# Optimization experiments

Measured on AMD Instinct MI355X. Metric: run time of the kernel, lower is better.

Reference implementation:

```python
import jax, jax.numpy as jnp
import numpy as np

B, T, DM, DH, DD, V, K = 2, 512, 1024, 4096, 4, 32000, 8
THR = 0.25
EPS = 1e-5
IGN = -100


def setup_inputs() -> dict:
    key = jax.random.key(0)
    ks = jax.random.split(key, 12)
    s = 0.02
    return {
        "H": jax.random.normal(ks[0], (B, T, DM), jnp.float32),
        "input_ids": jax.random.randint(ks[1], (B, T), 0, V),
        "attention_mask": jax.random.randint(ks[2], (B, T), 0, 2),
        "labels": jax.random.randint(ks[3], (B, T), 0, V),
        "emb": s * jax.random.normal(ks[4], (V, DM), jnp.float32),
        "depth_emb": s * jax.random.normal(ks[5], (DD, DM), jnp.float32),
        "ln_g": jnp.ones((DM,), jnp.float32),
        "ln_b": jnp.zeros((DM,), jnp.float32),
        "W1": s * jax.random.normal(ks[6], (DM, DH), jnp.float32),
        "b1": jnp.zeros((DH,), jnp.float32),
        "W2": s * jax.random.normal(ks[7], (DH, DM), jnp.float32),
        "b2": jnp.zeros((DM,), jnp.float32),
        "Wq": s * jax.random.normal(ks[8], (DM, V), jnp.float32),
        "bq": jnp.zeros((V,), jnp.float32),
        "Wb": s * jax.random.normal(ks[9], (DM, 1), jnp.float32),
        "bb": jnp.zeros((1,), jnp.float32),
    }


def _forward(H, input_ids, attention_mask, labels, emb, depth_emb, ln_g, ln_b, W1, b1, W2, b2, Wq, bq, Wb, bb):
    mask = attention_mask.astype(bool)  # (B,T)
    E = emb[input_ids]  # (B,T,DM)
    # draft state: broadcast over depth dim
    S = H[:, :, None, :] + E[:, :, None, :] + depth_emb[None, None]  # (B,T,DD,DM)
    mu = S.mean(-1, keepdims=True)
    var = ((S - mu) ** 2).mean(-1, keepdims=True)  # biased var, as torch LayerNorm
    S = (S - mu) * jax.lax.rsqrt(var + EPS) * ln_g + ln_b
    S = jax.nn.gelu(S @ W1 + b1, approximate=False) @ W2 + b2
    q = S @ Wq + bq  # (B,T,DD,V)
    beta = (S @ Wb + bb)[..., 0]  # (B,T,DD)
    q = jnp.where(mask[:, :, None, None], q, 0.0)
    beta = jnp.where(mask[:, :, None], beta, 0.0)
    # future labels for D depths (small fixed loop over DD)
    targets = jnp.full((B, T, DD), IGN, jnp.int32)
    valid = jnp.zeros((B, T, DD), bool)
    for d in range(1, DD + 1):
        v = mask[:, : T - d] & mask[:, d:]
        valid = valid.at[:, : T - d, d - 1].set(v)
        targets = targets.at[:, : T - d, d - 1].set(
            jnp.where(v, labels[:, d:].astype(jnp.int32), IGN))
    # token CE over valid positions (masked mean)
    logp = jax.nn.log_softmax(q, axis=-1)
    safe = jnp.where(valid, targets, 0)
    nll = -jnp.take_along_axis(logp, safe[..., None], axis=-1)[..., 0]
    cnt = valid.sum()
    L_q = jnp.where(cnt > 0, (nll * valid).sum() / jnp.maximum(cnt, 1).astype(q.dtype), jnp.zeros((), q.dtype))
    # BCE-with-logits on beta, averaged over valid source positions
    bce = jnp.logaddexp(0.0, beta) - beta * valid.astype(beta.dtype)
    src = valid.any(-1, keepdims=True)
    denom = jnp.maximum(src.sum(), 1).astype(beta.dtype)
    L_beta = (bce * src).sum() / denom
    return q, beta, L_q + L_beta


def reference(H, input_ids, attention_mask, labels, emb, depth_emb, ln_g, ln_b, W1, b1, W2, b2, Wq, bq, Wb, bb):
    q, beta, loss = _forward(H, input_ids, attention_mask, labels, emb, depth_emb,
                             ln_g, ln_b, W1, b1, W2, b2, Wq, bq, Wb, bb)
    # dynamic_branch_width
    sigma = jax.nn.sigmoid(beta)
    k = jnp.clip(jnp.ceil(sigma * float(K)).astype(jnp.int32), 1, K)
    k = jnp.where(sigma >= THR, k, 0)
    k = jnp.where(attention_mask.astype(bool)[:, :, None], k, 0)
    return q, beta, k, loss
```

## Files before the change

kernel.cpp:

```cpp
#include <hip/hip_runtime.h>
#include <math.h>

#define B_ 2
#define T_ 512
#define DM_ 1024
#define DH_ 4096
#define DD_ 4
#define V_ 32000
#define M_ 4096
#define BT_ 1024
#define NCHUNK3_ 125
#define PCH_ 128

typedef __attribute__((ext_vector_type(8))) unsigned short ushort8_t;
typedef __attribute__((ext_vector_type(4))) unsigned short ushort4_t;
typedef __attribute__((ext_vector_type(8))) __bf16 bf16x8;
typedef __attribute__((ext_vector_type(4))) float f32x4;

__device__ __forceinline__ unsigned short f2bf(float x) {
  union { float f; unsigned u; } v; v.f = x;
  unsigned r = v.u + 0x7fffu + ((v.u >> 16) & 1u);
  return (unsigned short)(r >> 16);
}
__device__ __forceinline__ float bf2f(unsigned short h) {
  union { unsigned u; float f; } v; v.u = ((unsigned)h) << 16; return v.f;
}

__device__ __forceinline__ void gload16(const void* g, void* l) {
  __builtin_amdgcn_global_load_lds(
      (const __attribute__((address_space(1))) void*)g,
      (__attribute__((address_space(3))) void*)l, 16, 0, 0);
}

template<int ROWS, int NWAVE>
__device__ __forceinline__ void stage_swz(const unsigned short* __restrict__ src, int ld,
                                          unsigned short* lds, int wid, int lane) {
  constexpr int NLOAD = ROWS / (16 * NWAVE);
  const int rl = lane >> 2;
  const int slot = (lane & 3) ^ ((lane >> 3) & 3);
  #pragma unroll
  for (int i = 0; i < NLOAD; ++i) {
    const int rbase = (i * NWAVE + wid) * 16;
    gload16(src + (size_t)(rbase + rl) * ld + slot * 8, lds + rbase * 32);
  }
}

__device__ __forceinline__ bf16x8 ldfrag(const unsigned short* t, int r, int s) {
  return __builtin_bit_cast(bf16x8,
      *(const ushort8_t*)&t[r * 32 + ((s ^ ((r >> 1) & 3)) * 8)]);
}

__device__ __forceinline__ float block_sum256(float v, float* sh) {
  #pragma unroll
  for (int o = 32; o >= 1; o >>= 1) v += __shfl_down(v, o);
  int lane = threadIdx.x & 63, wid = threadIdx.x >> 6;
  if (lane == 0) sh[wid] = v;
  __syncthreads();
  float t = sh[0] + sh[1] + sh[2] + sh[3];
  __syncthreads();
  return t;
}

__global__ __launch_bounds__(256) void transpose_split_kernel(
    const float* __restrict__ in, int R, int C,
    unsigned short* __restrict__ out_hi, unsigned short* __restrict__ out_lo)
{
  __shared__ float tile[32][33];
  int c0 = blockIdx.x * 32, r0 = blockIdx.y * 32;
  int tx = threadIdx.x & 31, ty = threadIdx.x >> 5;
  #pragma unroll
  for (int i = 0; i < 4; ++i)
    tile[ty + i * 8][tx] = in[(size_t)(r0 + ty + i * 8) * C + c0 + tx];
  __syncthreads();
  #pragma unroll
  for (int i = 0; i < 4; ++i) {
    int orow = c0 + ty + i * 8;
    int ocol = r0 + tx;
    float v = tile[tx][ty + i * 8];
    unsigned short h = f2bf(v);
    out_hi[(size_t)orow * R + ocol] = h;
    if (out_lo) out_lo[(size_t)orow * R + ocol] = f2bf(v - bf2f(h));
  }
}

__global__ __launch_bounds__(256) void embed_ln_kernel(
    const float* __restrict__ H, const int* __restrict__ ids,
    const float* __restrict__ emb, const float* __restrict__ demb,
    const float* __restrict__ g, const float* __restrict__ be,
    unsigned short* __restrict__ Xhi, unsigned short* __restrict__ Xlo)
{
  __shared__ float sh[8];
  int m = blockIdx.x, tid = threadIdx.x;
  int bt = m >> 2, d = m & 3;
  int id = ids[bt];
  float4 x  = ((const float4*)(H   + (size_t)bt * DM_))[tid];
  float4 e  = ((const float4*)(emb + (size_t)id * DM_))[tid];
  float4 de = ((const float4*)(demb + (size_t)d * DM_))[tid];
  float v0 = x.x + e.x + de.x, v1 = x.y + e.y + de.y;
  float v2 = x.z + e.z + de.z, v3 = x.w + e.w + de.w;
  float mu = block_sum256((v0 + v1) + (v2 + v3), sh) * (1.0f / DM_);
  float d0 = v0 - mu, d1v = v1 - mu, d2 = v2 - mu, d3 = v3 - mu;
  float var = block_sum256((d0 * d0 + d1v * d1v) + (d2 * d2 + d3 * d3), sh) * (1.0f / DM_);
  float rs = rsqrtf(var + 1e-5f);
  float4 gg  = ((const float4*)g)[tid];
  float4 bb4 = ((const float4*)be)[tid];
  float y0 = d0 * rs * gg.x + bb4.x;
  float y1 = d1v * rs * gg.y + bb4.y;
  float y2 = d2 * rs * gg.z + bb4.z;
  float y3 = d3 * rs * gg.w + bb4.w;
  unsigned short h0 = f2bf(y0), h1 = f2bf(y1), h2 = f2bf(y2), h3 = f2bf(y3);
  ushort4_t hv = {h0, h1, h2, h3};
  ushort4_t lv = {f2bf(y0 - bf2f(h0)), f2bf(y1 - bf2f(h1)), f2bf(y2 - bf2f(h2)), f2bf(y3 - bf2f(h3))};
  size_t base = (size_t)m * DM_ + tid * 4;
  *(ushort4_t*)&Xhi[base] = hv;
  *(ushort4_t*)&Xlo[base] = lv;
}

__global__ __launch_bounds__(64) void w2b_kernel(
    const float* __restrict__ W2, const float* __restrict__ Wb,
    const float* __restrict__ b2, const float* __restrict__ bb,
    float* __restrict__ w2b)
{
  int j = blockIdx.x, lane = threadIdx.x;
  const float* rowp = (j < DH_) ? (W2 + (size_t)j * DM_) : b2;
  const float4* r4 = (const float4*)rowp;
  const float4* w4 = (const float4*)Wb;
  float s = 0.0f;
  for (int i = lane; i < DM_ / 4; i += 64) {
    float4 a = r4[i], w = w4[i];
    s += a.x * w.x + a.y * w.y + a.z * w.z + a.w * w.w;
  }
  #pragma unroll
  for (int o = 32; o >= 1; o >>= 1) s += __shfl_down(s, o);
  if (lane == 0) w2b[j] = (j < DH_) ? s : (s + bb[0]);
}

template<int BM, int BN, int NWAVE, int WN,
         bool SPLIT, bool GELU, bool CEPART, bool BETAPART, bool NTC>
__global__ __launch_bounds__(NWAVE * 64, 2) void gemm3p_kernel(
    const unsigned short* __restrict__ Ahi, const unsigned short* __restrict__ Alo,
    const unsigned short* __restrict__ Bhi, const unsigned short* __restrict__ Blo,
    const float* __restrict__ bias, int Ndim, int Kdim,
    float* __restrict__ Cf, unsigned short* __restrict__ Chi, unsigned short* __restrict__ Clo,
    const int* __restrict__ rowmask,
    const float* __restrict__ w2bv, float* __restrict__ bpart,
    float* __restrict__ pmax, float* __restrict__ psum)
{
  constexpr int WM = NWAVE / WN;
  constexpr int MI = (BM / WM) / 16;
  constexpr int NI = (BN / WN) / 16;
  constexpr int AW = BM * 32;
  constexpr int BW = BN * 32;
  constexpr int BUFW = (SPLIT ? 2 : 1) * (AW + BW);
  constexpr int LPS = (SPLIT ? 2 : 1) * (BM / (16 * NWAVE) + BN / (16 * NWAVE));
  static_assert(LPS == 4, "vmcnt(4) assumes exactly 4 loads per wave per stage");
  __shared__ __align__(16) unsigned short smem[3 * BUFW];

  const int m0 = blockIdx.x * BM, n0 = blockIdx.y * BN;
  const int tid = threadIdx.x, lane = tid & 63, wid = tid >> 6;
  const int wr = wid / WN, wc = wid % WN;
  const int lrow = lane & 15, q4 = lane >> 4;
  const int wrb = wr * (BM / WM), wcb = wc * (BN / WN);

  const unsigned short* Ab  = Ahi + (size_t)m0 * Kdim;
  const unsigned short* Bb  = Bhi + (size_t)n0 * Kdim;
  const unsigned short* Alb = SPLIT ? (Alo + (size_t)m0 * Kdim) : nullptr;
  const unsigned short* Blb = SPLIT ? (Blo + (size_t)n0 * Kdim) : nullptr;

  f32x4 acc[MI][NI] = {};
  const int NT = Kdim / 32;

  auto stageAll = [&](unsigned short* base, int kt) {
    const int ko = kt * 32;
    stage_swz<BM, NWAVE>(Ab + ko, Kdim, base, wid, lane);
    stage_swz<BN, NWAVE>(Bb + ko, Kdim, base + AW, wid, lane);
    if constexpr (SPLIT) {
      stage_swz<BM, NWAVE>(Alb + ko, Kdim, base + AW + BW, wid, lane);
      stage_swz<BN, NWAVE>(Blb + ko, Kdim, base + 2 * AW + BW, wid, lane);
    }
  };

  unsigned short* p0 = smem;
  unsigned short* p1 = smem + BUFW;
  unsigned short* p2 = smem + 2 * BUFW;

  stageAll(p0, 0);
  stageAll(p1, 1);

  for (int kt = 0; kt < NT; ++kt) {
    if (kt + 1 < NT) asm volatile("s_waitcnt vmcnt(4)" ::: "memory");
    else             asm volatile("s_waitcnt vmcnt(0)" ::: "memory");
    __builtin_amdgcn_s_barrier();
    __builtin_amdgcn_sched_barrier(0);
    if (kt + 2 < NT) stageAll(p2, kt + 2);
    __builtin_amdgcn_sched_barrier(0);

    const unsigned short* sA = p0;
    const unsigned short* sB = p0 + AW;
    bf16x8 bh[NI], bl[NI];
    #pragma unroll
    for (int ni = 0; ni < NI; ++ni) {
      bh[ni] = ldfrag(sB, wcb + ni * 16 + lrow, q4);
      if constexpr (SPLIT) bl[ni] = ldfrag(sB + AW + BW, wcb + ni * 16 + lrow, q4);
    }
    #pragma unroll
    for (int mi = 0; mi < MI; ++mi) {
      const int r = wrb + mi * 16 + lrow;
      bf16x8 ah = ldfrag(sA, r, q4);
      bf16x8 al;
      if constexpr (SPLIT) al = ldfrag(sA + AW + BW, r, q4);
      #pragma unroll
      for (int ni = 0; ni < NI; ++ni) {
        acc[mi][ni] = __builtin_amdgcn_mfma_f32_16x16x32_bf16(ah, bh[ni], acc[mi][ni], 0, 0, 0);
        if constexpr (SPLIT) {
          acc[mi][ni] = __builtin_amdgcn_mfma_f32_16x16x32_bf16(ah, bl[ni], acc[mi][ni], 0, 0, 0);
          acc[mi][ni] = __builtin_amdgcn_mfma_f32_16x16x32_bf16(al, bh[ni], acc[mi][ni], 0, 0, 0);
        }
      }
    }
    unsigned short* t = p0; p0 = p1; p1 = p2; p2 = t;
  }
  __syncthreads();

  #pragma unroll
  for (int mi = 0; mi < MI; ++mi)
    #pragma unroll
    for (int ni = 0; ni < NI; ++ni) {
      const int col = n0 + wcb + ni * 16 + lrow;
      const float bv = bias ? bias[col] : 0.0f;
      #pragma unroll
      for (int r2 = 0; r2 < 4; ++r2) {
        const int gm = m0 + wrb + mi * 16 + q4 * 4 + r2;
        float v = acc[mi][ni][r2] + bv;
        if constexpr (GELU) v = 0.5f * v * (1.0f + erff(v * 0.70710678118654752440f));
        if (rowmask) v *= (rowmask[gm >> 2] ? 1.0f : 0.0f);
        acc[mi][ni][r2] = v;
        const size_t idx = (size_t)gm * Ndim + col;
        if (Cf) {
          if constexpr (NTC) __builtin_nontemporal_store(v, &Cf[idx]);
          else Cf[idx] = v;
        }
        if (Chi) {
          unsigned short h = f2bf(v);
          Chi[idx] = h;
          if (Clo) Clo[idx] = f2bf(v - bf2f(h));
        }
      }
    }

  float* red = (float*)smem;

  if constexpr (CEPART) {
    #pragma unroll
    for (int mi = 0; mi < MI; ++mi)
      #pragma unroll
      for (int r2 = 0; r2 < 4; ++r2) {
        float mx = -3.4e38f;
        #pragma unroll
        for (int ni = 0; ni < NI; ++ni) mx = fmaxf(mx, acc[mi][ni][r2]);
        #pragma unroll
        for (int o = 1; o < 16; o <<= 1) mx = fmaxf(mx, __shfl_xor(mx, o));
        float sm = 0.0f;
        #pragma unroll
        for (int ni = 0; ni < NI; ++ni) sm += expf(acc[mi][ni][r2] - mx);
        #pragma unroll
        for (int o = 1; o < 16; o <<= 1) sm += __shfl_xor(sm, o);
        if (lrow == 0) {
          const int rowL = wrb + mi * 16 + q4 * 4 + r2;
          red[(rowL * WN + wc) * 2 + 0] = mx;
          red[(rowL * WN + wc) * 2 + 1] = sm;
        }
      }
    __syncthreads();
    for (int r = tid; r < BM; r += NWAVE * 64) {
      float mg = -3.4e38f, sg = 0.0f;
      #pragma unroll
      for (int w = 0; w < WN; ++w) {
        float mw = red[(r * WN + w) * 2 + 0], sw = red[(r * WN + w) * 2 + 1];
        float nm = fmaxf(mg, mw);
        sg = sg * expf(mg - nm) + sw * expf(mw - nm);
        mg = nm;
      }
      pmax[(size_t)(m0 + r) * PCH_ + blockIdx.y] = mg;
      psum[(size_t)(m0 + r) * PCH_ + blockIdx.y] = sg;
    }
  }

  if constexpr (BETAPART) {
    #pragma unroll
    for (int mi = 0; mi < MI; ++mi)
      #pragma unroll
      for (int r2 = 0; r2 < 4; ++r2) {
        float s = 0.0f;
        #pragma unroll
        for (int ni = 0; ni < NI; ++ni)
          s += acc[mi][ni][r2] * w2bv[n0 + wcb + ni * 16 + lrow];
        #pragma unroll
        for (int o = 1; o < 16; o <<= 1) s += __shfl_xor(s, o);
        if (lrow == 0)
          red[(wrb + mi * 16 + q4 * 4 + r2) * WN + wc] = s;
      }
    __syncthreads();
    for (int r = tid; r < BM; r += NWAVE * 64) {
      float s = 0.0f;
      #pragma unroll
      for (int w = 0; w < WN; ++w) s += red[r * WN + w];
      bpart[(size_t)(m0 + r) * 32 + blockIdx.y] = s;
    }
  }
}

__global__ __launch_bounds__(64) void beta_k_kernel(
    const float* __restrict__ bpart, const float* __restrict__ w2b,
    const int* __restrict__ mask,
    float* __restrict__ beta_out, float* __restrict__ k_out,
    float* __restrict__ bce, int* __restrict__ validf)
{
  int m = blockIdx.x, lane = threadIdx.x;
  float s = (lane < 32) ? bpart[(size_t)m * 32 + lane] : 0.0f;
  #pragma unroll
  for (int o = 32; o >= 1; o >>= 1) s += __shfl_down(s, o);
  if (lane == 0) {
    int bt = m >> 2, d1 = (m & 3) + 1;
    float beta = s + w2b[DH_];
    int mv = mask[bt];
    float bm = mv ? beta : 0.0f;
    int t = bt % T_;
    int valid = (t + d1 < T_) && mv && mask[bt + d1];
    beta_out[m] = bm;
    float sp = fmaxf(bm, 0.0f) + log1pf(expf(-fabsf(bm)));
    bce[m] = sp - (valid ? bm : 0.0f);
    validf[m] = valid;
    float sig = 1.0f / (1.0f + expf(-bm));
    int kk = (int)ceilf(sig * 8.0f);
    kk = kk < 1 ? 1 : (kk > 8 ? 8 : kk);
    if (!(sig >= 0.25f)) kk = 0;
    if (!mv) kk = 0;
    k_out[m] = (float)kk;
  }
}

__global__ __launch_bounds__(64) void ce_reduce_kernel(
    const float* __restrict__ pmax, const float* __restrict__ psum,
    const float* __restrict__ q, const int* __restrict__ validf,
    const int* __restrict__ labels, float* __restrict__ nll)
{
  int m = blockIdx.x, lane = threadIdx.x;
  if (!validf[m]) { if (lane == 0) nll[m] = 0.0f; return; }
  float ml = -3.4e38f, sl = 0.0f;
  for (int j = lane; j < NCHUNK3_; j += 64) {
    float mj = pmax[(size_t)m * PCH_ + j], sj = psum[(size_t)m * PCH_ + j];
    float nm = fmaxf(ml, mj);
    sl = sl * expf(ml - nm) + sj * expf(mj - nm);
    ml = nm;
  }
  #pragma unroll
  for (int o = 32; o >= 1; o >>= 1) {
    float mo = __shfl_xor(ml, o), so = __shfl_xor(sl, o);
    float nm = fmaxf(ml, mo);
    sl = sl * expf(ml - nm) + so * expf(mo - nm);
    ml = nm;
  }
  if (lane == 0) {
    int bt = m >> 2, d1 = (m & 3) + 1;
    float qt = q[(size_t)m * V_ + labels[bt + d1]];
    nll[m] = -(qt - ml - logf(sl));
  }
}

__global__ __launch_bounds__(256) void loss_kernel(
    const float* __restrict__ nll, const int* __restrict__ validf,
    const float* __restrict__ bce, float* __restrict__ loss_out)
{
  __shared__ float sh[8];
  int tid = threadIdx.x;
  float snll = 0.0f, fcnt = 0.0f, sbce = 0.0f, fnsrc = 0.0f;
  for (int m = tid; m < M_; m += 256) { snll += nll[m]; fcnt += (float)validf[m]; }
  for (int bt = tid; bt < BT_; bt += 256) {
    int base = bt * 4;
    int src = validf[base] | validf[base + 1] | validf[base + 2] | validf[base + 3];
    if (src) { sbce += bce[base] + bce[base + 1] + bce[base + 2] + bce[base + 3]; fnsrc += 1.0f; }
  }
  snll = block_sum256(snll, sh);
  fcnt = block_sum256(fcnt, sh);
  sbce = block_sum256(sbce, sh);
  fnsrc = block_sum256(fnsrc, sh);
  if (tid == 0) {
    float Lq = fcnt > 0.0f ? snll / fcnt : 0.0f;
    float Lb = sbce / fmaxf(fnsrc, 1.0f);
    loss_out[0] = Lq + Lb;
  }
}

extern "C" void kernel_launch(void* const* d_in, const int* in_sizes, int n_in,
                              void* d_out, int out_size, void* d_ws, size_t ws_size,
                              hipStream_t stream) {
  const float* H    = (const float*)d_in[0];
  const int*   ids  = (const int*)d_in[1];
  const int*   mask = (const int*)d_in[2];
  const int*   labels = (const int*)d_in[3];
  const float* emb  = (const float*)d_in[4];
  const float* demb = (const float*)d_in[5];
  const float* ln_g = (const float*)d_in[6];
  const float* ln_b = (const float*)d_in[7];
  const float* W1   = (const float*)d_in[8];
  const float* b1   = (const float*)d_in[9];
  const float* W2   = (const float*)d_in[10];
  const float* b2   = (const float*)d_in[11];
  const float* Wq   = (const float*)d_in[12];
  const float* bq   = (const float*)d_in[13];
  const float* Wb   = (const float*)d_in[14];
  const float* bb   = (const float*)d_in[15];

  char* ws = (char*)d_ws; size_t off = 0;
  auto walloc = [&](size_t bytes) -> void* {
    void* p = ws + off; off = (off + bytes + 255) & ~(size_t)255; return p;
  };
  unsigned short* W1t_hi = (unsigned short*)walloc((size_t)DH_ * DM_ * 2);
  unsigned short* W1t_lo = (unsigned short*)walloc((size_t)DH_ * DM_ * 2);
  unsigned short* W2t_hi = (unsigned short*)walloc((size_t)DM_ * DH_ * 2);
  unsigned short* Wqt_hi = (unsigned short*)walloc((size_t)V_ * DM_ * 2);
  unsigned short* Xhi    = (unsigned short*)walloc((size_t)M_ * DM_ * 2);
  unsigned short* Xlo    = (unsigned short*)walloc((size_t)M_ * DM_ * 2);
  unsigned short* S2hi   = (unsigned short*)walloc((size_t)M_ * DM_ * 2);
  float* w2b    = (float*)walloc((DH_ + 1) * 4);
  float* bpart  = (float*)walloc((size_t)M_ * 32 * 4);
  float* pmax   = (float*)walloc((size_t)M_ * PCH_ * 4);
  float* psum   = (float*)walloc((size_t)M_ * PCH_ * 4);
  float* nll    = (float*)walloc(M_ * 4);
  float* bcev   = (float*)walloc(M_ * 4);
  int*   validf = (int*)walloc(M_ * 4);

  float* q_out    = (float*)d_out;
  float* beta_out = q_out + (size_t)M_ * V_;
  float* k_out    = beta_out + M_;
  float* loss_out = k_out + M_;
  unsigned short* act_hi = (unsigned short*)d_out;
  unsigned short* act_lo = act_hi + (size_t)M_ * DH_;

  transpose_split_kernel<<<dim3(DH_ / 32, DM_ / 32), 256, 0, stream>>>(W1, DM_, DH_, W1t_hi, W1t_lo);
  transpose_split_kernel<<<dim3(DM_ / 32, DH_ / 32), 256, 0, stream>>>(W2, DH_, DM_, W2t_hi, nullptr);
  transpose_split_kernel<<<dim3(V_ / 32, DM_ / 32), 256, 0, stream>>>(Wq, DM_, V_, Wqt_hi, nullptr);
  embed_ln_kernel<<<M_, 256, 0, stream>>>(H, ids, emb, demb, ln_g, ln_b, Xhi, Xlo);
  w2b_kernel<<<DH_ + 1, 64, 0, stream>>>(W2, Wb, b2, bb, w2b);
  gemm3p_kernel<128, 128, 8, 4, true, true, false, true, false>
      <<<dim3(M_ / 128, DH_ / 128), 512, 0, stream>>>(
      Xhi, Xlo, W1t_hi, W1t_lo, b1, DH_, DM_, nullptr, act_hi, act_lo, nullptr,
      w2b, bpart, nullptr, nullptr);
  beta_k_kernel<<<M_, 64, 0, stream>>>(bpart, w2b, mask, beta_out, k_out, bcev, validf);
  gemm3p_kernel<128, 128, 4, 2, false, false, false, false, false>
      <<<dim3(M_ / 128, DM_ / 128), 256, 0, stream>>>(
      act_hi, nullptr, W2t_hi, nullptr, b2, DM_, DH_, nullptr, S2hi, nullptr, nullptr,
      nullptr, nullptr, nullptr, nullptr);
  gemm3p_kernel<256, 256, 8, 4, false, false, true, false, true>
      <<<dim3(M_ / 256, V_ / 256), 512, 0, stream>>>(
      S2hi, nullptr, Wqt_hi, nullptr, bq, V_, DM_, q_out, nullptr, nullptr, mask,
      nullptr, nullptr, pmax, psum);
  ce_reduce_kernel<<<M_, 64, 0, stream>>>(pmax, psum, q_out, validf, labels, nll);
  loss_kernel<<<1, 256, 0, stream>>>(nll, validf, bcev, loss_out);
}
```

Before: 1.392 ms.

## Add 8-phase ping-pong GEMM kernel with split-precision as concatenated K

Adds a new 256x256-tile GEMM kernel that interleaves LDS fragment loads, global-to-LDS staging and MFMA groups across eight barrier-separated phases, using s_setprio to favour MFMA issue. It is used for the vocabulary projection and for the first MLP layer. The first layer's three-product split-bf16 scheme is now written as one GEMM over a threefold-longer K dimension built from segment pointers (Xhi·W1hi, Xhi·W1lo, Xlo·W1hi) rather than three MFMAs per step. The beta partial-sum reduction is narrowed to 16 column blocks to match the wider tile. The aim is better MFMA utilisation and latency hiding, at the cost of a rigid hand-written schedule with many barriers that assumes a fixed 1024-wide K segment.

```diff
diff --git a/kernel.cpp b/kernel.cpp
--- a/kernel.cpp
+++ b/kernel.cpp
@@ -11,6 +11,7 @@
 #define BT_ 1024
 #define NCHUNK3_ 125
 #define PCH_ 128
+#define NB1_ 16
 
 typedef __attribute__((ext_vector_type(8))) unsigned short ushort8_t;
 typedef __attribute__((ext_vector_type(4))) unsigned short ushort4_t;
@@ -30,24 +31,6 @@
   __builtin_amdgcn_global_load_lds(
       (const __attribute__((address_space(1))) void*)g,
       (__attribute__((address_space(3))) void*)l, 16, 0, 0);
-}
-
-template<int ROWS, int NWAVE>
-__device__ __forceinline__ void stage_swz(const unsigned short* __restrict__ src, int ld,
-                                          unsigned short* lds, int wid, int lane) {
-  constexpr int NLOAD = ROWS / (16 * NWAVE);
-  const int rl = lane >> 2;
-  const int slot = (lane & 3) ^ ((lane >> 3) & 3);
-  #pragma unroll
-  for (int i = 0; i < NLOAD; ++i) {
-    const int rbase = (i * NWAVE + wid) * 16;
-    gload16(src + (size_t)(rbase + rl) * ld + slot * 8, lds + rbase * 32);
-  }
-}
-
-__device__ __forceinline__ bf16x8 ldfrag(const unsigned short* t, int r, int s) {
-  return __builtin_bit_cast(bf16x8,
-      *(const ushort8_t*)&t[r * 32 + ((s ^ ((r >> 1) & 3)) * 8)]);
 }
 
 __device__ __forceinline__ float block_sum256(float v, float* sh) {
@@ -60,6 +43,7 @@
   __syncthreads();
   return t;
 }
+
 
 __global__ __launch_bounds__(256) void transpose_split_kernel(
     const float* __restrict__ in, int R, int C,
@@ -135,25 +119,39 @@
   if (lane == 0) w2b[j] = (j < DH_) ? s : (s + bb[0]);
 }
 
-template<int BM, int BN, int NWAVE, int WN,
-         bool SPLIT, bool GELU, bool CEPART, bool BETAPART, bool NTC>
+
+template<int ROWS, int NWAVE>
+__device__ __forceinline__ void stage_swz(const unsigned short* __restrict__ src, int ld,
+                                          unsigned short* lds, int wid, int lane) {
+  constexpr int NLOAD = ROWS / (16 * NWAVE);
+  const int rl = lane >> 2;
+  const int slot = (lane & 3) ^ ((lane >> 3) & 3);
+  #pragma unroll
+  for (int i = 0; i < NLOAD; ++i) {
+    const int rbase = (i * NWAVE + wid) * 16;
+    gload16(src + (size_t)(rbase + rl) * ld + slot * 8, lds + rbase * 32);
+  }
+}
+__device__ __forceinline__ bf16x8 ldfrag(const unsigned short* t, int r, int s) {
+  return __builtin_bit_cast(bf16x8,
+      *(const ushort8_t*)&t[r * 32 + ((s ^ ((r >> 1) & 3)) * 8)]);
+}
+
+template<int BM, int BN, int NWAVE, int WN>
 __global__ __launch_bounds__(NWAVE * 64, 2) void gemm3p_kernel(
-    const unsigned short* __restrict__ Ahi, const unsigned short* __restrict__ Alo,
-    const unsigned short* __restrict__ Bhi, const unsigned short* __restrict__ Blo,
+    const unsigned short* __restrict__ Ahi,
+    const unsigned short* __restrict__ Bhi,
     const float* __restrict__ bias, int Ndim, int Kdim,
-    float* __restrict__ Cf, unsigned short* __restrict__ Chi, unsigned short* __restrict__ Clo,
-    const int* __restrict__ rowmask,
-    const float* __restrict__ w2bv, float* __restrict__ bpart,
-    float* __restrict__ pmax, float* __restrict__ psum)
+    unsigned short* __restrict__ Chi)
 {
   constexpr int WM = NWAVE / WN;
   constexpr int MI = (BM / WM) / 16;
   constexpr int NI = (BN / WN) / 16;
   constexpr int AW = BM * 32;
   constexpr int BW = BN * 32;
-  constexpr int BUFW = (SPLIT ? 2 : 1) * (AW + BW);
-  constexpr int LPS = (SPLIT ? 2 : 1) * (BM / (16 * NWAVE) + BN / (16 * NWAVE));
-  static_assert(LPS == 4, "vmcnt(4) assumes exactly 4 loads per wave per stage");
+  constexpr int BUFW = AW + BW;
+  constexpr int LPS = (BM / (16 * NWAVE) + BN / (16 * NWAVE));
+  static_assert(LPS * NWAVE * 16 == BM + BN, "");
   __shared__ __align__(16) unsigned short smem[3 * BUFW];
 
   const int m0 = blockIdx.x * BM, n0 = blockIdx.y * BN;
@@ -162,10 +160,8 @@
   const int lrow = lane & 15, q4 = lane >> 4;
   const int wrb = wr * (BM / WM), wcb = wc * (BN / WN);
 
-  const unsigned short* Ab  = Ahi + (size_t)m0 * Kdim;
-  const unsigned short* Bb  = Bhi + (size_t)n0 * Kdim;
-  const unsigned short* Alb = SPLIT ? (Alo + (size_t)m0 * Kdim) : nullptr;
-  const unsigned short* Blb = SPLIT ? (Blo + (size_t)n0 * Kdim) : nullptr;
+  const unsigned short* Ab = Ahi + (size_t)m0 * Kdim;
+  const unsigned short* Bb = Bhi + (size_t)n0 * Kdim;
 
   f32x4 acc[MI][NI] = {};
   const int NT = Kdim / 32;
@@ -174,16 +170,11 @@
     const int ko = kt * 32;
     stage_swz<BM, NWAVE>(Ab + ko, Kdim, base, wid, lane);
     stage_swz<BN, NWAVE>(Bb + ko, Kdim, base + AW, wid, lane);
-    if constexpr (SPLIT) {
-      stage_swz<BM, NWAVE>(Alb + ko, Kdim, base + AW + BW, wid, lane);
-      stage_swz<BN, NWAVE>(Blb + ko, Kdim, base + 2 * AW + BW, wid, lane);
-    }
   };
 
   unsigned short* p0 = smem;
   unsigned short* p1 = smem + BUFW;
   unsigned short* p2 = smem + 2 * BUFW;
-
   stageAll(p0, 0);
   stageAll(p1, 1);
 
@@ -194,38 +185,187 @@
     __builtin_amdgcn_sched_barrier(0);
     if (kt + 2 < NT) stageAll(p2, kt + 2);
     __builtin_amdgcn_sched_barrier(0);
-
     const unsigned short* sA = p0;
     const unsigned short* sB = p0 + AW;
-    bf16x8 bh[NI], bl[NI];
-    #pragma unroll
-    for (int ni = 0; ni < NI; ++ni) {
-      bh[ni] = ldfrag(sB, wcb + ni * 16 + lrow, q4);
-      if constexpr (SPLIT) bl[ni] = ldfrag(sB + AW + BW, wcb + ni * 16 + lrow, q4);
-    }
+    bf16x8 bh[NI];
+    #pragma unroll
+    for (int ni = 0; ni < NI; ++ni) bh[ni] = ldfrag(sB, wcb + ni * 16 + lrow, q4);
     #pragma unroll
     for (int mi = 0; mi < MI; ++mi) {
-      const int r = wrb + mi * 16 + lrow;
-      bf16x8 ah = ldfrag(sA, r, q4);
-      bf16x8 al;
-      if constexpr (SPLIT) al = ldfrag(sA + AW + BW, r, q4);
-      #pragma unroll
-      for (int ni = 0; ni < NI; ++ni) {
+      bf16x8 ah = ldfrag(sA, wrb + mi * 16 + lrow, q4);
+      #pragma unroll
+      for (int ni = 0; ni < NI; ++ni)
         acc[mi][ni] = __builtin_amdgcn_mfma_f32_16x16x32_bf16(ah, bh[ni], acc[mi][ni], 0, 0, 0);
-        if constexpr (SPLIT) {
-          acc[mi][ni] = __builtin_amdgcn_mfma_f32_16x16x32_bf16(ah, bl[ni], acc[mi][ni], 0, 0, 0);
-          acc[mi][ni] = __builtin_amdgcn_mfma_f32_16x16x32_bf16(al, bh[ni], acc[mi][ni], 0, 0, 0);
-        }
-      }
     }
     unsigned short* t = p0; p0 = p1; p1 = p2; p2 = t;
   }
-  __syncthreads();
 
   #pragma unroll
   for (int mi = 0; mi < MI; ++mi)
     #pragma unroll
     for (int ni = 0; ni < NI; ++ni) {
+      const int col = n0 + wcb + ni * 16 + lrow;
+      const float bv = bias ? bias[col] : 0.0f;
+      #pragma unroll
+      for (int r2 = 0; r2 < 4; ++r2) {
+        const int gm = m0 + wrb + mi * 16 + q4 * 4 + r2;
+        float v = acc[mi][ni][r2] + bv;
+        Chi[(size_t)gm * Ndim + col] = f2bf(v);
+      }
+    }
+}
+
+template<bool GELU, bool CEPART, bool BETAPART, bool NTC>
+__global__ __launch_bounds__(512, 2) void gemm8p_kernel(
+    const unsigned short* __restrict__ A0s, const unsigned short* __restrict__ A1s,
+    const unsigned short* __restrict__ A2s,
+    const unsigned short* __restrict__ B0s, const unsigned short* __restrict__ B1s,
+    const unsigned short* __restrict__ B2s,
+    const float* __restrict__ bias, int Ndim, int Kdim,
+    float* __restrict__ Cf, unsigned short* __restrict__ Chi, unsigned short* __restrict__ Clo,
+    const int* __restrict__ rowmask,
+    const float* __restrict__ w2bv, float* __restrict__ bpart,
+    float* __restrict__ pmax, float* __restrict__ psum)
+{
+  __shared__ __align__(16) unsigned short smem[65536];
+
+  const int m0 = blockIdx.x * 256, n0 = blockIdx.y * 256;
+  const int tid = threadIdx.x, lane = tid & 63, wid = tid >> 6;
+  const int wr = wid >> 2, wc = wid & 3;
+  const int lrow = lane & 15, q4 = lane >> 4;
+  const int wrb = wr * 128, wcb = wc * 64;
+  const int NKT = Kdim >> 6, NIT = NKT >> 1, HT_END = NKT << 2;
+
+  const int rs = lane >> 3;
+  const int cs8 = ((lane & 7) ^ rs) * 8;
+  const int sx0 = (q4 ^ (lrow & 7)) * 8;
+  const int sx1 = ((4 + q4) ^ (lrow & 7)) * 8;
+  const int abase = (wrb + lrow) * 64;
+  const int bbase = 16384 + (wcb + lrow) * 64;
+
+  auto ld8 = [&](int off) {
+    return __builtin_bit_cast(bf16x8, *(const ushort8_t*)&smem[off]);
+  };
+  auto stage_ht = [&](int h) {
+    if (h >= HT_END) return;
+    const int kt = h >> 2, part = h & 3;
+    const int seg = kt >> 4, kc = (kt & 15) << 6;
+    const unsigned short* mat;
+    if (part & 2) mat = (seg == 0) ? A0s : ((seg == 1) ? A1s : A2s);
+    else          mat = (seg == 0) ? B0s : ((seg == 1) ? B1s : B2s);
+    const int row = ((part & 2) ? m0 : n0) + ((part & 1) << 7) + wid * 16 + rs;
+    const unsigned short* g = mat + (size_t)row * 1024 + kc + cs8;
+    unsigned short* d = smem + ((kt & 1) << 15)
+                      + ((part & 2) ? ((part & 1) << 13) : (16384 + ((part & 1) << 13)))
+                      + wid * 1024;
+    gload16(g, d);
+    gload16(g + (size_t)(8 * 1024), d + 512);
+  };
+
+  f32x4 acc[8][4] = {};
+  bf16x8 a[4][2], b0[2][2], b1[2][2];
+
+  int hnext = 6;
+  #pragma unroll
+  for (int h = 0; h < 6; ++h) stage_ht(h);
+  asm volatile("s_waitcnt vmcnt(4)" ::: "memory");
+  __builtin_amdgcn_s_barrier();
+
+  for (int i = 0; i < NIT; ++i) {
+    #pragma unroll
+    for (int half = 0; half < 2; ++half) {
+      const int kb = half << 15;
+      if (half == 0 || i + 1 < NIT) { asm volatile("s_waitcnt vmcnt(4)" ::: "memory"); }
+      else                          { asm volatile("s_waitcnt vmcnt(0)" ::: "memory"); }
+      #pragma unroll
+      for (int mi = 0; mi < 4; ++mi) {
+        a[mi][0] = ld8(kb + abase + mi * 1024 + sx0);
+        a[mi][1] = ld8(kb + abase + mi * 1024 + sx1);
+      }
+      #pragma unroll
+      for (int ni = 0; ni < 2; ++ni) {
+        b0[ni][0] = ld8(kb + bbase + ni * 1024 + sx0);
+        b0[ni][1] = ld8(kb + bbase + ni * 1024 + sx1);
+      }
+      stage_ht(hnext++);
+      __builtin_amdgcn_sched_barrier(0);
+      __builtin_amdgcn_s_barrier();
+      asm volatile("s_waitcnt lgkmcnt(0)" ::: "memory");
+      __builtin_amdgcn_sched_barrier(0);
+      __builtin_amdgcn_s_setprio(1);
+      #pragma unroll
+      for (int mi = 0; mi < 4; ++mi)
+        #pragma unroll
+        for (int ni = 0; ni < 2; ++ni) {
+          acc[mi][ni] = __builtin_amdgcn_mfma_f32_16x16x32_bf16(a[mi][0], b0[ni][0], acc[mi][ni], 0, 0, 0);
+          acc[mi][ni] = __builtin_amdgcn_mfma_f32_16x16x32_bf16(a[mi][1], b0[ni][1], acc[mi][ni], 0, 0, 0);
+        }
+      __builtin_amdgcn_s_setprio(0);
+      __builtin_amdgcn_sched_barrier(0);
+      __builtin_amdgcn_s_barrier();
+      #pragma unroll
+      for (int ni = 0; ni < 2; ++ni) {
+        b1[ni][0] = ld8(kb + bbase + (2 + ni) * 1024 + sx0);
+        b1[ni][1] = ld8(kb + bbase + (2 + ni) * 1024 + sx1);
+      }
+      stage_ht(hnext++);
+      __builtin_amdgcn_sched_barrier(0);
+      __builtin_amdgcn_s_barrier();
+      asm volatile("s_waitcnt lgkmcnt(0)" ::: "memory");
+      __builtin_amdgcn_sched_barrier(0);
+      __builtin_amdgcn_s_setprio(1);
+      #pragma unroll
+      for (int mi = 0; mi < 4; ++mi)
+        #pragma unroll
+        for (int ni = 0; ni < 2; ++ni) {
+          acc[mi][2 + ni] = __builtin_amdgcn_mfma_f32_16x16x32_bf16(a[mi][0], b1[ni][0], acc[mi][2 + ni], 0, 0, 0);
+          acc[mi][2 + ni] = __builtin_amdgcn_mfma_f32_16x16x32_bf16(a[mi][1], b1[ni][1], acc[mi][2 + ni], 0, 0, 0);
+        }
+      __builtin_amdgcn_s_setprio(0);
+      __builtin_amdgcn_sched_barrier(0);
+      __builtin_amdgcn_s_barrier();
+      #pragma unroll
+      for (int mi = 0; mi < 4; ++mi) {
+        a[mi][0] = ld8(kb + abase + (4 + mi) * 1024 + sx0);
+        a[mi][1] = ld8(kb + abase + (4 + mi) * 1024 + sx1);
+      }
+      stage_ht(hnext++);
+      __builtin_amdgcn_sched_barrier(0);
+      __builtin_amdgcn_s_barrier();
+      asm volatile("s_waitcnt lgkmcnt(0)" ::: "memory");
+      __builtin_amdgcn_sched_barrier(0);
+      __builtin_amdgcn_s_setprio(1);
+      #pragma unroll
+      for (int mi = 0; mi < 4; ++mi)
+        #pragma unroll
+        for (int ni = 0; ni < 2; ++ni) {
+          acc[4 + mi][2 + ni] = __builtin_amdgcn_mfma_f32_16x16x32_bf16(a[mi][0], b1[ni][0], acc[4 + mi][2 + ni], 0, 0, 0);
+          acc[4 + mi][2 + ni] = __builtin_amdgcn_mfma_f32_16x16x32_bf16(a[mi][1], b1[ni][1], acc[4 + mi][2 + ni], 0, 0, 0);
+        }
+      __builtin_amdgcn_s_setprio(0);
+      __builtin_amdgcn_sched_barrier(0);
+      __builtin_amdgcn_s_barrier();
+      stage_ht(hnext++);
+      __builtin_amdgcn_sched_barrier(0);
+      __builtin_amdgcn_s_barrier();
+      __builtin_amdgcn_s_setprio(1);
+      #pragma unroll
+      for (int mi = 0; mi < 4; ++mi)
+        #pragma unroll
+        for (int ni = 0; ni < 2; ++ni) {
+          acc[4 + mi][ni] = __builtin_amdgcn_mfma_f32_16x16x32_bf16(a[mi][0], b0[ni][0], acc[4 + mi][ni], 0, 0, 0);
+          acc[4 + mi][ni] = __builtin_amdgcn_mfma_f32_16x16x32_bf16(a[mi][1], b0[ni][1], acc[4 + mi][ni], 0, 0, 0);
+        }
+      __builtin_amdgcn_s_setprio(0);
+      __builtin_amdgcn_sched_barrier(0);
+      __builtin_amdgcn_s_barrier();
+    }
+  }
+
+  #pragma unroll
+  for (int mi = 0; mi < 8; ++mi)
+    #pragma unroll
+    for (int ni = 0; ni < 4; ++ni) {
       const int col = n0 + wcb + ni * 16 + lrow;
       const float bv = bias ? bias[col] : 0.0f;
       #pragma unroll
@@ -251,32 +391,33 @@
   float* red = (float*)smem;
 
   if constexpr (CEPART) {
-    #pragma unroll
-    for (int mi = 0; mi < MI; ++mi)
+    __syncthreads();
+    #pragma unroll
+    for (int mi = 0; mi < 8; ++mi)
       #pragma unroll
       for (int r2 = 0; r2 < 4; ++r2) {
         float mx = -3.4e38f;
         #pragma unroll
-        for (int ni = 0; ni < NI; ++ni) mx = fmaxf(mx, acc[mi][ni][r2]);
+        for (int ni = 0; ni < 4; ++ni) mx = fmaxf(mx, acc[mi][ni][r2]);
         #pragma unroll
         for (int o = 1; o < 16; o <<= 1) mx = fmaxf(mx, __shfl_xor(mx, o));
         float sm = 0.0f;
         #pragma unroll
-        for (int ni = 0; ni < NI; ++ni) sm += expf(acc[mi][ni][r2] - mx);
+        for (int ni = 0; ni < 4; ++ni) sm += expf(acc[mi][ni][r2] - mx);
         #pragma unroll
         for (int o = 1; o < 16; o <<= 1) sm += __shfl_xor(sm, o);
         if (lrow == 0) {
           const int rowL = wrb + mi * 16 + q4 * 4 + r2;
-          red[(rowL * WN + wc) * 2 + 0] = mx;
-          red[(rowL * WN + wc) * 2 + 1] = sm;
+          red[(rowL * 4 + wc) * 2 + 0] = mx;
+          red[(rowL * 4 + wc) * 2 + 1] = sm;
         }
       }
     __syncthreads();
-    for (int r = tid; r < BM; r += NWAVE * 64) {
+    for (int r = tid; r < 256; r += 512) {
       float mg = -3.4e38f, sg = 0.0f;
       #pragma unroll
-      for (int w = 0; w < WN; ++w) {
-        float mw = red[(r * WN + w) * 2 + 0], sw = red[(r * WN + w) * 2 + 1];
+      for (int w = 0; w < 4; ++w) {
+        float mw = red[(r * 4 + w) * 2 + 0], sw = red[(r * 4 + w) * 2 + 1];
         float nm = fmaxf(mg, mw);
         sg = sg * expf(mg - nm) + sw * expf(mw - nm);
         mg = nm;
@@ -287,28 +428,28 @@
   }
 
   if constexpr (BETAPART) {
-    #pragma unroll
-    for (int mi = 0; mi < MI; ++mi)
+    __syncthreads();
+    #pragma unroll
+    for (int mi = 0; mi < 8; ++mi)
       #pragma unroll
       for (int r2 = 0; r2 < 4; ++r2) {
         float s = 0.0f;
         #pragma unroll
-        for (int ni = 0; ni < NI; ++ni)
+        for (int ni = 0; ni < 4; ++ni)
           s += acc[mi][ni][r2] * w2bv[n0 + wcb + ni * 16 + lrow];
         #pragma unroll
         for (int o = 1; o < 16; o <<= 1) s += __shfl_xor(s, o);
         if (lrow == 0)
-          red[(wrb + mi * 16 + q4 * 4 + r2) * WN + wc] = s;
+          red[(wrb + mi * 16 + q4 * 4 + r2) * 4 + wc] = s;
       }
     __syncthreads();
-    for (int r = tid; r < BM; r += NWAVE * 64) {
-      float s = 0.0f;
-      #pragma unroll
-      for (int w = 0; w < WN; ++w) s += red[r * WN + w];
+    for (int r = tid; r < 256; r += 512) {
+      float s = red[r * 4 + 0] + red[r * 4 + 1] + red[r * 4 + 2] + red[r * 4 + 3];
       bpart[(size_t)(m0 + r) * 32 + blockIdx.y] = s;
     }
   }
 }
+
 
 __global__ __launch_bounds__(64) void beta_k_kernel(
     const float* __restrict__ bpart, const float* __restrict__ w2b,
@@ -317,7 +458,7 @@
     float* __restrict__ bce, int* __restrict__ validf)
 {
   int m = blockIdx.x, lane = threadIdx.x;
-  float s = (lane < 32) ? bpart[(size_t)m * 32 + lane] : 0.0f;
+  float s = (lane < NB1_) ? bpart[(size_t)m * 32 + lane] : 0.0f;
   #pragma unroll
   for (int o = 32; o >= 1; o >>= 1) s += __shfl_down(s, o);
   if (lane == 0) {
@@ -443,19 +584,15 @@
   transpose_split_kernel<<<dim3(V_ / 32, DM_ / 32), 256, 0, stream>>>(Wq, DM_, V_, Wqt_hi, nullptr);
   embed_ln_kernel<<<M_, 256, 0, stream>>>(H, ids, emb, demb, ln_g, ln_b, Xhi, Xlo);
   w2b_kernel<<<DH_ + 1, 64, 0, stream>>>(W2, Wb, b2, bb, w2b);
-  gemm3p_kernel<128, 128, 8, 4, true, true, false, true, false>
-      <<<dim3(M_ / 128, DH_ / 128), 512, 0, stream>>>(
-      Xhi, Xlo, W1t_hi, W1t_lo, b1, DH_, DM_, nullptr, act_hi, act_lo, nullptr,
-      w2b, bpart, nullptr, nullptr);
+  gemm8p_kernel<true, false, true, false><<<dim3(M_ / 256, DH_ / 256), 512, 0, stream>>>(
+      Xhi, Xhi, Xlo, W1t_hi, W1t_lo, W1t_hi, b1, DH_, 3 * DM_,
+      nullptr, act_hi, act_lo, nullptr, w2b, bpart, nullptr, nullptr);
   beta_k_kernel<<<M_, 64, 0, stream>>>(bpart, w2b, mask, beta_out, k_out, bcev, validf);
-  gemm3p_kernel<128, 128, 4, 2, false, false, false, false, false>
-      <<<dim3(M_ / 128, DM_ / 128), 256, 0, stream>>>(
-      act_hi, nullptr, W2t_hi, nullptr, b2, DM_, DH_, nullptr, S2hi, nullptr, nullptr,
-      nullptr, nullptr, nullptr, nullptr);
-  gemm3p_kernel<256, 256, 8, 4, false, false, true, false, true>
-      <<<dim3(M_ / 256, V_ / 256), 512, 0, stream>>>(
-      S2hi, nullptr, Wqt_hi, nullptr, bq, V_, DM_, q_out, nullptr, nullptr, mask,
-      nullptr, nullptr, pmax, psum);
+  gemm3p_kernel<128, 128, 4, 2><<<dim3(M_ / 128, DM_ / 128), 256, 0, stream>>>(
+      act_hi, W2t_hi, b2, DM_, DH_, S2hi);
+  gemm8p_kernel<false, true, false, true><<<dim3(M_ / 256, V_ / 256), 512, 0, stream>>>(
+      S2hi, S2hi, S2hi, Wqt_hi, Wqt_hi, Wqt_hi, bq, V_, DM_,
+      q_out, nullptr, nullptr, mask, nullptr, nullptr, pmax, psum);
   ce_reduce_kernel<<<M_, 64, 0, stream>>>(pmax, psum, q_out, validf, labels, nll);
   loss_kernel<<<1, 256, 0, stream>>>(nll, validf, bcev, loss_out);
 }
```

Result: slower. 1.728 ms (+24.2%).
